# Kernel tuning notes

Measured on AMD Instinct MI355X. Metric: run time of the kernel, lower is better.

The kernel has to match this reference:

```python
import jax, jax.numpy as jnp
import numpy as np

NOISE_STD = 0.01  # noise_std init arg


def setup_inputs() -> dict:
    key = jax.random.key(0)
    k1, k2, k3, k4, k5 = jax.random.split(key, 5)
    B, C, H, W = 32, 256, 56, 56
    x = jax.random.normal(k1, (B, C, H, W), dtype=jnp.float32)
    H_real = jax.random.normal(k2, (B, C, C), dtype=jnp.float32)
    H_imag = jax.random.normal(k3, (B, C, C), dtype=jnp.float32)
    noise_real = jax.random.normal(k4, (B, C, H, W), dtype=jnp.float32)
    noise_imag = jax.random.normal(k5, (B, C, H, W), dtype=jnp.float32)
    return {"x": x, "H_real": H_real, "H_imag": H_imag,
            "noise_real": noise_real, "noise_imag": noise_imag}


def reference(x, H_real, H_imag, noise_real, noise_imag):
    # x: (B,C,H,W) real. Per-batch complex MIMO channel Hc = (Hr + i*Hi)/sqrt(2*C).
    # Since x has zero imaginary part, y = Hc @ x splits into two real GEMMs.
    C = x.shape[1]
    scale = 1.0 / jnp.sqrt(jnp.asarray(2.0 * C, dtype=x.dtype))
    yr = jnp.einsum('bij,bjhw->bihw', H_real, x) * scale + noise_real * NOISE_STD
    yi = jnp.einsum('bij,bjhw->bihw', H_imag, x) * scale + noise_imag * NOISE_STD
    # output_mode == 'magnitude' -> |y|
    return jnp.sqrt(yr * yr + yi * yi)
```

## Files before the change

kernel.cpp:

```cpp
#include <hip/hip_runtime.h>
#include <hip/hip_bf16.h>
#include <math.h>


#define NBATCH 32
#define NC 256
#define NP 3136
#define BM 128
#define BN 64
#define BK 32
#define NBN 49
#define NKI 8

typedef __attribute__((ext_vector_type(8))) short short8;
typedef __attribute__((ext_vector_type(4))) float f32x4;

static __device__ __forceinline__ void gload16(const void* g, void* l) {
  __builtin_amdgcn_global_load_lds(
      (const __attribute__((address_space(1))) void*)g,
      (__attribute__((address_space(3))) void*)l, 16, 0, 0);
}

static __device__ __forceinline__ unsigned short bfr(float f) {
  __hip_bfloat16 h = __float2bfloat16(f);
  return *reinterpret_cast<unsigned short*>(&h);
}

__global__ __launch_bounds__(256)
void perm_h_kernel(const float* __restrict__ hr, const float* __restrict__ hi,
                   unsigned short* __restrict__ ws)
{
  const int blk   = blockIdx.x;
  const int kt    = blk & 7;
  const int b2m   = blk >> 3;
  const int plane = threadIdx.x >> 7;
  const int row   = threadIdx.x & 127;
  const int b     = b2m >> 1;
  const int bm    = b2m & 1;

  const float* src = (plane ? hi : hr)
      + ((size_t)b * NC + bm * 128 + row) * NC + kt * 32;
  unsigned short* dst = ws + ((size_t)(b2m * 8 + kt) * 2 + plane) * 4096 + row * 8;

  #pragma unroll
  for (int fq = 0; fq < 4; ++fq) {
    const float4 v0 = *reinterpret_cast<const float4*>(src + fq * 8);
    const float4 v1 = *reinterpret_cast<const float4*>(src + fq * 8 + 4);
    union { uint4 v; unsigned short u[8]; } o;
    o.u[0] = bfr(v0.x); o.u[1] = bfr(v0.y); o.u[2] = bfr(v0.z); o.u[3] = bfr(v0.w);
    o.u[4] = bfr(v1.x); o.u[5] = bfr(v1.y); o.u[6] = bfr(v1.z); o.u[7] = bfr(v1.w);
    *reinterpret_cast<uint4*>(dst + fq * 1024) = o.v;
  }
}

template<int PRE>
__global__ __launch_bounds__(512, 4)
void rayleigh_main(const float* __restrict__ xg,
                   const float* __restrict__ Hrg,
                   const float* __restrict__ Hig,
                   const unsigned short* __restrict__ Hperm,
                   const float* __restrict__ nrg,
                   const float* __restrict__ nig,
                   float* __restrict__ outg)
{
  __shared__ float x_lds[2][BK * BN];
  __shared__ unsigned short hr_lds[2][4096];
  __shared__ unsigned short hi_lds[2][4096];

  const int raw = blockIdx.x;
  const int v   = (raw & 7) * 392 + (raw >> 3);
  const int b   = v / 98;
  const int r2  = v - b * 98;
  const int bm  = r2 / 49;
  const int bn  = r2 - bm * 49;

  const int tid  = threadIdx.x;
  const int lane = tid & 63;
  const int wave = tid >> 6;
  const int wm   = wave >> 2;
  const int wn   = wave & 3;
  const int fr   = lane & 15;
  const int fq   = lane >> 4;

  const float* xsrc = xg + (size_t)b * NC * NP + (size_t)bn * BN;
  const size_t hrowbase = (size_t)b * NC + bm * BM;
  const size_t hpbase = (size_t)((b * 2 + bm) * 8);

  auto stage = [&](int t, int buf) {
    {
      const int C16 = wave * 64 + lane;
      const int k   = C16 >> 4;
      const int cp  = C16 & 15;
      const int fqk = k >> 3;
      const int cl  = cp ^ (((fqk & 1) << 2) | (fqk >> 1));
      const float* src = xsrc + (size_t)(t * BK + k) * NP + cl * 4;
      gload16(src, (char*)x_lds[buf] + wave * 1024);
    }
    if constexpr (PRE) {
      #pragma unroll
      for (int i = 0; i < 2; ++i) {
        const int c     = wave * 2 + i;
        const int plane = c >> 3;
        const int fqc   = (c >> 1) & 3;
        const int half  = c & 1;
        unsigned short* hl = plane ? hi_lds[buf] : hr_lds[buf];
        const unsigned short* src = Hperm
            + ((hpbase + t) * 2 + plane) * 4096
            + fqc * 1024 + (half * 64 + lane) * 8;
        gload16(src, (char*)hl + fqc * 2048 + half * 1024);
      }
    }
  };

  f32x4 accR[4], accI[4];
  #pragma unroll
  for (int m = 0; m < 4; ++m) {
    accR[m] = (f32x4){0.f, 0.f, 0.f, 0.f};
    accI[m] = (f32x4){0.f, 0.f, 0.f, 0.f};
  }
  float nrv[4][4], niv[4][4];

  const size_t obase = ((size_t)b * NC + bm * BM + wm * 64 + fq * 4) * NP
                     + (size_t)bn * BN + wn * 16 + fr;
  const int xork = ((fq & 1) << 6) | ((fq >> 1) << 4);
  const int pcol = ((wn * 16 + fr) << 2) ^ xork;

  stage(0, 0);

  #pragma unroll
  for (int t = 0; t < NKI; ++t) {
    __syncthreads();
    if (t + 1 < NKI) stage(t + 1, (t + 1) & 1);

    {
      const int m = t >> 1, rb = (t & 1) * 2;
      #pragma unroll
      for (int r = 0; r < 2; ++r) {
        const size_t idx = obase + (size_t)(m * 16 + rb + r) * NP;
        nrv[m][rb + r] = __builtin_nontemporal_load(nrg + idx);
        niv[m][rb + r] = __builtin_nontemporal_load(nig + idx);
      }
    }

    const char* xbuf = (const char*)x_lds[t & 1];
    union { short8 s; unsigned short u[8]; } u;
    #pragma unroll
    for (int j = 0; j < 8; ++j) {
      const float f = *reinterpret_cast<const float*>(xbuf + ((fq * 8 + j) << 8) + pcol);
      u.u[j] = bfr(f);
    }
    const short8 xb = u.s;

    #pragma unroll
    for (int m = 0; m < 4; ++m) {
      const int row = wm * 64 + m * 16 + fr;
      short8 ar, ai;
      if constexpr (PRE) {
        ar = *reinterpret_cast<const short8*>(&hr_lds[t & 1][fq * 1024 + row * 8]);
        ai = *reinterpret_cast<const short8*>(&hi_lds[t & 1][fq * 1024 + row * 8]);
      } else {
        const float* p1 = Hrg + (hrowbase + row) * NC + t * BK + fq * 8;
        const float* p2 = Hig + (hrowbase + row) * NC + t * BK + fq * 8;
        const float4 v0 = *reinterpret_cast<const float4*>(p1);
        const float4 v1 = *reinterpret_cast<const float4*>(p1 + 4);
        const float4 w0 = *reinterpret_cast<const float4*>(p2);
        const float4 w1 = *reinterpret_cast<const float4*>(p2 + 4);
        union { short8 s; unsigned short uu[8]; } a1, a2;
        a1.uu[0] = bfr(v0.x); a1.uu[1] = bfr(v0.y); a1.uu[2] = bfr(v0.z); a1.uu[3] = bfr(v0.w);
        a1.uu[4] = bfr(v1.x); a1.uu[5] = bfr(v1.y); a1.uu[6] = bfr(v1.z); a1.uu[7] = bfr(v1.w);
        a2.uu[0] = bfr(w0.x); a2.uu[1] = bfr(w0.y); a2.uu[2] = bfr(w0.z); a2.uu[3] = bfr(w0.w);
        a2.uu[4] = bfr(w1.x); a2.uu[5] = bfr(w1.y); a2.uu[6] = bfr(w1.z); a2.uu[7] = bfr(w1.w);
        ar = a1.s; ai = a2.s;
      }
      accR[m] = __builtin_amdgcn_mfma_f32_16x16x32_bf16(ar, xb, accR[m], 0, 0, 0);
      accI[m] = __builtin_amdgcn_mfma_f32_16x16x32_bf16(ai, xb, accI[m], 0, 0, 0);
    }
  }

  const float scale = 0.04419417382415922f;
  const float nstd  = 0.01f;
  #pragma unroll
  for (int m = 0; m < 4; ++m)
    #pragma unroll
    for (int r = 0; r < 4; ++r) {
      const size_t idx = obase + (size_t)(m * 16 + r) * NP;
      const float yr = accR[m][r] * scale + nrv[m][r] * nstd;
      const float yi = accI[m][r] * scale + niv[m][r] * nstd;
      outg[idx] = sqrtf(yr * yr + yi * yi);
    }
}

extern "C" void kernel_launch(void* const* d_in, const int* in_sizes, int n_in,
                              void* d_out, int out_size, void* d_ws, size_t ws_size,
                              hipStream_t stream) {
  const float* x  = (const float*)d_in[0];
  const float* Hr = (const float*)d_in[1];
  const float* Hi = (const float*)d_in[2];
  const float* nr = (const float*)d_in[3];
  const float* ni = (const float*)d_in[4];
  float* out = (float*)d_out;

  const size_t HN = (size_t)NBATCH * NC * NC;

  if (ws_size >= HN * 2 * sizeof(unsigned short)) {
    unsigned short* hperm = (unsigned short*)d_ws;
    hipLaunchKernelGGL(perm_h_kernel, dim3(512), dim3(256), 0, stream, Hr, Hi, hperm);
    hipLaunchKernelGGL((rayleigh_main<1>), dim3(NBATCH * 2 * NBN), dim3(512), 0, stream,
                       x, Hr, Hi, hperm, nr, ni, out);
  } else {
    hipLaunchKernelGGL((rayleigh_main<0>), dim3(NBATCH * 2 * NBN), dim3(512), 0, stream,
                       x, Hr, Hi, (const unsigned short*)nullptr, nr, ni, out);
  }
}
```

Baseline: 107.2 us.

## Load full x tile to LDS upfront and stream H from global into registers

Replaces the double-buffered per-K-step LDS staging of x and H with a single upfront load of the whole 256x64 x tile into LDS (64KB) and one barrier. H fragments are now read straight from global memory (L2-cached, prepacked bf16) into registers with an A/B register ping-pong. Noise loads move from interleaved inside the K loop to the epilogue and drop the nontemporal hint. This removes the per-step barriers, but the larger LDS footprint lowers occupancy and the noise load latency is now exposed at the end.

```diff
diff --git a/kernel.cpp b/kernel.cpp
--- a/kernel.cpp
+++ b/kernel.cpp
@@ -63,9 +63,7 @@
                    const float* __restrict__ nig,
                    float* __restrict__ outg)
 {
-  __shared__ float x_lds[2][BK * BN];
-  __shared__ unsigned short hr_lds[2][4096];
-  __shared__ unsigned short hi_lds[2][4096];
+  __shared__ float x_lds[NC * BN];
 
   const int raw = blockIdx.x;
   const int v   = (raw & 7) * 392 + (raw >> 3);
@@ -84,33 +82,17 @@
 
   const float* xsrc = xg + (size_t)b * NC * NP + (size_t)bn * BN;
   const size_t hrowbase = (size_t)b * NC + bm * BM;
-  const size_t hpbase = (size_t)((b * 2 + bm) * 8);
-
-  auto stage = [&](int t, int buf) {
-    {
-      const int C16 = wave * 64 + lane;
-      const int k   = C16 >> 4;
-      const int cp  = C16 & 15;
-      const int fqk = k >> 3;
-      const int cl  = cp ^ (((fqk & 1) << 2) | (fqk >> 1));
-      const float* src = xsrc + (size_t)(t * BK + k) * NP + cl * 4;
-      gload16(src, (char*)x_lds[buf] + wave * 1024);
-    }
-    if constexpr (PRE) {
-      #pragma unroll
-      for (int i = 0; i < 2; ++i) {
-        const int c     = wave * 2 + i;
-        const int plane = c >> 3;
-        const int fqc   = (c >> 1) & 3;
-        const int half  = c & 1;
-        unsigned short* hl = plane ? hi_lds[buf] : hr_lds[buf];
-        const unsigned short* src = Hperm
-            + ((hpbase + t) * 2 + plane) * 4096
-            + fqc * 1024 + (half * 64 + lane) * 8;
-        gload16(src, (char*)hl + fqc * 2048 + half * 1024);
-      }
-    }
-  };
+  const size_t hpbase   = (size_t)((b * 2 + bm) * 8);
+
+  #pragma unroll
+  for (int i = 0; i < 8; ++i) {
+    const int C16 = (i * 8 + wave) * 64 + lane;
+    const int k   = C16 >> 4;
+    const int cp  = C16 & 15;
+    const int fqk = (k >> 3) & 3;
+    const int cl  = cp ^ (((fqk & 1) << 2) | (fqk >> 1));
+    gload16(xsrc + (size_t)k * NP + cl * 4, (char*)x_lds + (i * 8 + wave) * 1024);
+  }
 
   f32x4 accR[4], accI[4];
   #pragma unroll
@@ -118,74 +100,83 @@
     accR[m] = (f32x4){0.f, 0.f, 0.f, 0.f};
     accI[m] = (f32x4){0.f, 0.f, 0.f, 0.f};
   }
-  float nrv[4][4], niv[4][4];
-
-  const size_t obase = ((size_t)b * NC + bm * BM + wm * 64 + fq * 4) * NP
-                     + (size_t)bn * BN + wn * 16 + fr;
+
   const int xork = ((fq & 1) << 6) | ((fq >> 1) << 4);
   const int pcol = ((wn * 16 + fr) << 2) ^ xork;
-
-  stage(0, 0);
-
-  #pragma unroll
-  for (int t = 0; t < NKI; ++t) {
-    __syncthreads();
-    if (t + 1 < NKI) stage(t + 1, (t + 1) & 1);
-
-    {
-      const int m = t >> 1, rb = (t & 1) * 2;
-      #pragma unroll
-      for (int r = 0; r < 2; ++r) {
-        const size_t idx = obase + (size_t)(m * 16 + rb + r) * NP;
-        nrv[m][rb + r] = __builtin_nontemporal_load(nrg + idx);
-        niv[m][rb + r] = __builtin_nontemporal_load(nig + idx);
-      }
-    }
-
-    const char* xbuf = (const char*)x_lds[t & 1];
-    union { short8 s; unsigned short u[8]; } u;
-    #pragma unroll
-    for (int j = 0; j < 8; ++j) {
-      const float f = *reinterpret_cast<const float*>(xbuf + ((fq * 8 + j) << 8) + pcol);
-      u.u[j] = bfr(f);
-    }
-    const short8 xb = u.s;
-
+  const int hfo  = fq * 1024 + (wm * 64 + fr) * 8;
+
+  auto loadH = [&](int t, short8 (&ar)[4], short8 (&ai)[4]) {
     #pragma unroll
     for (int m = 0; m < 4; ++m) {
-      const int row = wm * 64 + m * 16 + fr;
-      short8 ar, ai;
       if constexpr (PRE) {
-        ar = *reinterpret_cast<const short8*>(&hr_lds[t & 1][fq * 1024 + row * 8]);
-        ai = *reinterpret_cast<const short8*>(&hi_lds[t & 1][fq * 1024 + row * 8]);
+        const unsigned short* p = Hperm + ((hpbase + t) * 2) * 4096 + hfo + m * 128;
+        ar[m] = *reinterpret_cast<const short8*>(p);
+        ai[m] = *reinterpret_cast<const short8*>(p + 4096);
       } else {
-        const float* p1 = Hrg + (hrowbase + row) * NC + t * BK + fq * 8;
-        const float* p2 = Hig + (hrowbase + row) * NC + t * BK + fq * 8;
+        const float* p1 = Hrg + (hrowbase + wm * 64 + m * 16 + fr) * NC + t * 32 + fq * 8;
+        const float* p2 = Hig + (hrowbase + wm * 64 + m * 16 + fr) * NC + t * 32 + fq * 8;
         const float4 v0 = *reinterpret_cast<const float4*>(p1);
         const float4 v1 = *reinterpret_cast<const float4*>(p1 + 4);
         const float4 w0 = *reinterpret_cast<const float4*>(p2);
         const float4 w1 = *reinterpret_cast<const float4*>(p2 + 4);
-        union { short8 s; unsigned short uu[8]; } a1, a2;
-        a1.uu[0] = bfr(v0.x); a1.uu[1] = bfr(v0.y); a1.uu[2] = bfr(v0.z); a1.uu[3] = bfr(v0.w);
-        a1.uu[4] = bfr(v1.x); a1.uu[5] = bfr(v1.y); a1.uu[6] = bfr(v1.z); a1.uu[7] = bfr(v1.w);
-        a2.uu[0] = bfr(w0.x); a2.uu[1] = bfr(w0.y); a2.uu[2] = bfr(w0.z); a2.uu[3] = bfr(w0.w);
-        a2.uu[4] = bfr(w1.x); a2.uu[5] = bfr(w1.y); a2.uu[6] = bfr(w1.z); a2.uu[7] = bfr(w1.w);
-        ar = a1.s; ai = a2.s;
+        union { short8 s; unsigned short u[8]; } a1, a2;
+        a1.u[0] = bfr(v0.x); a1.u[1] = bfr(v0.y); a1.u[2] = bfr(v0.z); a1.u[3] = bfr(v0.w);
+        a1.u[4] = bfr(v1.x); a1.u[5] = bfr(v1.y); a1.u[6] = bfr(v1.z); a1.u[7] = bfr(v1.w);
+        a2.u[0] = bfr(w0.x); a2.u[1] = bfr(w0.y); a2.u[2] = bfr(w0.z); a2.u[3] = bfr(w0.w);
+        a2.u[4] = bfr(w1.x); a2.u[5] = bfr(w1.y); a2.u[6] = bfr(w1.z); a2.u[7] = bfr(w1.w);
+        ar[m] = a1.s; ai[m] = a2.s;
       }
-      accR[m] = __builtin_amdgcn_mfma_f32_16x16x32_bf16(ar, xb, accR[m], 0, 0, 0);
-      accI[m] = __builtin_amdgcn_mfma_f32_16x16x32_bf16(ai, xb, accI[m], 0, 0, 0);
-    }
+    }
+  };
+
+  auto step = [&](int t, short8 (&ar)[4], short8 (&ai)[4]) {
+    union { short8 s; unsigned short u[8]; } u;
+    #pragma unroll
+    for (int j = 0; j < 8; ++j) {
+      const float f = *reinterpret_cast<const float*>(
+          (const char*)x_lds + ((t * 32 + fq * 8 + j) << 8) + pcol);
+      u.u[j] = bfr(f);
+    }
+    const short8 xb = u.s;
+    #pragma unroll
+    for (int m = 0; m < 4; ++m) {
+      accR[m] = __builtin_amdgcn_mfma_f32_16x16x32_bf16(ar[m], xb, accR[m], 0, 0, 0);
+      accI[m] = __builtin_amdgcn_mfma_f32_16x16x32_bf16(ai[m], xb, accI[m], 0, 0, 0);
+    }
+  };
+
+  short8 arA[4], aiA[4], arB[4], aiB[4];
+  loadH(0, arA, aiA);
+  __syncthreads();
+
+  #pragma unroll
+  for (int u2 = 0; u2 < 4; ++u2) {
+    loadH(2 * u2 + 1, arB, aiB);
+    step(2 * u2, arA, aiA);
+    if (u2 < 3) loadH(2 * u2 + 2, arA, aiA);
+    step(2 * u2 + 1, arB, aiB);
   }
 
   const float scale = 0.04419417382415922f;
   const float nstd  = 0.01f;
+  const size_t obase = ((size_t)b * NC + bm * BM + wm * 64 + fq * 4) * NP
+                     + (size_t)bn * BN + wn * 16 + fr;
+  float nrv[16], niv[16];
   #pragma unroll
   for (int m = 0; m < 4; ++m)
     #pragma unroll
     for (int r = 0; r < 4; ++r) {
       const size_t idx = obase + (size_t)(m * 16 + r) * NP;
-      const float yr = accR[m][r] * scale + nrv[m][r] * nstd;
-      const float yi = accI[m][r] * scale + niv[m][r] * nstd;
+      nrv[m * 4 + r] = nrg[idx];
+      niv[m * 4 + r] = nig[idx];
+    }
+  #pragma unroll
+  for (int m = 0; m < 4; ++m)
+    #pragma unroll
+    for (int r = 0; r < 4; ++r) {
+      const size_t idx = obase + (size_t)(m * 16 + r) * NP;
+      const float yr = accR[m][r] * scale + nrv[m * 4 + r] * nstd;
+      const float yi = accI[m][r] * scale + niv[m * 4 + r] * nstd;
       outg[idx] = sqrtf(yr * yr + yi * yi);
     }
 }
```

After: 133.0 us. 24.0% more time.

## Triple-buffer LDS staging with manual vmcnt waits and move noise loads to epilogue

Applied to the files above, without the earlier changes.

Switches the K-loop from double to triple buffering with a prefetch distance of two. It replaces __syncthreads with an explicit s_waitcnt vmcnt plus s_barrier so that in-flight global-to-LDS loads can overlap compute. The noise loads, which were interleaved into the K loop as nontemporal loads, now all issue in the epilogue as ordinary loads. This frees the loop's vmcnt accounting but exposes noise load latency at the end, and the extra LDS buffer may cut occupancy.

```diff
diff --git a/kernel.cpp b/kernel.cpp
--- a/kernel.cpp
+++ b/kernel.cpp
@@ -63,9 +63,9 @@
                    const float* __restrict__ nig,
                    float* __restrict__ outg)
 {
-  __shared__ float x_lds[2][BK * BN];
-  __shared__ unsigned short hr_lds[2][4096];
-  __shared__ unsigned short hi_lds[2][4096];
+  __shared__ float x_lds[3][BK * BN];
+  __shared__ unsigned short hr_lds[3][4096];
+  __shared__ unsigned short hi_lds[3][4096];
 
   const int raw = blockIdx.x;
   const int v   = (raw & 7) * 392 + (raw >> 3);
@@ -84,7 +84,7 @@
 
   const float* xsrc = xg + (size_t)b * NC * NP + (size_t)bn * BN;
   const size_t hrowbase = (size_t)b * NC + bm * BM;
-  const size_t hpbase = (size_t)((b * 2 + bm) * 8);
+  const size_t hpbase   = (size_t)((b * 2 + bm) * 8);
 
   auto stage = [&](int t, int buf) {
     {
@@ -118,7 +118,6 @@
     accR[m] = (f32x4){0.f, 0.f, 0.f, 0.f};
     accI[m] = (f32x4){0.f, 0.f, 0.f, 0.f};
   }
-  float nrv[4][4], niv[4][4];
 
   const size_t obase = ((size_t)b * NC + bm * BM + wm * 64 + fq * 4) * NP
                      + (size_t)bn * BN + wn * 16 + fr;
@@ -126,23 +125,21 @@
   const int pcol = ((wn * 16 + fr) << 2) ^ xork;
 
   stage(0, 0);
-
-  #pragma unroll
+  stage(1, 1);
+
   for (int t = 0; t < NKI; ++t) {
-    __syncthreads();
-    if (t + 1 < NKI) stage(t + 1, (t + 1) & 1);
-
-    {
-      const int m = t >> 1, rb = (t & 1) * 2;
-      #pragma unroll
-      for (int r = 0; r < 2; ++r) {
-        const size_t idx = obase + (size_t)(m * 16 + rb + r) * NP;
-        nrv[m][rb + r] = __builtin_nontemporal_load(nrg + idx);
-        niv[m][rb + r] = __builtin_nontemporal_load(nig + idx);
-      }
-    }
-
-    const char* xbuf = (const char*)x_lds[t & 1];
+    const int buf = t % 3;
+    if constexpr (PRE) {
+      if (t < NKI - 1) asm volatile("s_waitcnt vmcnt(3)" ::: "memory");
+      else             asm volatile("s_waitcnt vmcnt(0)" ::: "memory");
+      __builtin_amdgcn_s_barrier();
+      __builtin_amdgcn_sched_barrier(0);
+    } else {
+      __syncthreads();
+    }
+    if (t + 2 < NKI) stage(t + 2, (t + 2) % 3);
+
+    const char* xbuf = (const char*)x_lds[buf];
     union { short8 s; unsigned short u[8]; } u;
     #pragma unroll
     for (int j = 0; j < 8; ++j) {
@@ -156,11 +153,11 @@
       const int row = wm * 64 + m * 16 + fr;
       short8 ar, ai;
       if constexpr (PRE) {
-        ar = *reinterpret_cast<const short8*>(&hr_lds[t & 1][fq * 1024 + row * 8]);
-        ai = *reinterpret_cast<const short8*>(&hi_lds[t & 1][fq * 1024 + row * 8]);
+        ar = *reinterpret_cast<const short8*>(&hr_lds[buf][fq * 1024 + row * 8]);
+        ai = *reinterpret_cast<const short8*>(&hi_lds[buf][fq * 1024 + row * 8]);
       } else {
-        const float* p1 = Hrg + (hrowbase + row) * NC + t * BK + fq * 8;
-        const float* p2 = Hig + (hrowbase + row) * NC + t * BK + fq * 8;
+        const float* p1 = Hrg + (hrowbase + row) * NC + t * 32 + fq * 8;
+        const float* p2 = Hig + (hrowbase + row) * NC + t * 32 + fq * 8;
         const float4 v0 = *reinterpret_cast<const float4*>(p1);
         const float4 v1 = *reinterpret_cast<const float4*>(p1 + 4);
         const float4 w0 = *reinterpret_cast<const float4*>(p2);
@@ -179,13 +176,22 @@
 
   const float scale = 0.04419417382415922f;
   const float nstd  = 0.01f;
+  float nrv[16], niv[16];
   #pragma unroll
   for (int m = 0; m < 4; ++m)
     #pragma unroll
     for (int r = 0; r < 4; ++r) {
       const size_t idx = obase + (size_t)(m * 16 + r) * NP;
-      const float yr = accR[m][r] * scale + nrv[m][r] * nstd;
-      const float yi = accI[m][r] * scale + niv[m][r] * nstd;
+      nrv[m * 4 + r] = nrg[idx];
+      niv[m * 4 + r] = nig[idx];
+    }
+  #pragma unroll
+  for (int m = 0; m < 4; ++m)
+    #pragma unroll
+    for (int r = 0; r < 4; ++r) {
+      const size_t idx = obase + (size_t)(m * 16 + r) * NP;
+      const float yr = accR[m][r] * scale + nrv[m * 4 + r] * nstd;
+      const float yi = accI[m][r] * scale + niv[m * 4 + r] * nstd;
       outg[idx] = sqrtf(yr * yr + yi * yi);
     }
 }
```

Result: slower. 111.9 us (+4.4%).

## Cover full channel dimension per block so x tile is loaded once

Applied to the files above, without the earlier changes.

Enlarges the M tile from 128 to 256 rows so each block computes all output channels for its pixel tile. Each x tile is now read from global memory once instead of twice, and the grid shrinks to 1568 blocks. Each wave handles two N sub-tiles, which doubles the accumulators and the LDS for H. The noise loads move out of the K loop into the epilogue and output stores become nontemporal. The risk is fewer resident blocks from higher register and LDS use, and noise-load latency no longer hidden behind the main loop.

```diff
diff --git a/kernel.cpp b/kernel.cpp
--- a/kernel.cpp
+++ b/kernel.cpp
@@ -6,7 +6,7 @@
 #define NBATCH 32
 #define NC 256
 #define NP 3136
-#define BM 128
+#define BM 256
 #define BN 64
 #define BK 32
 #define NBN 49
@@ -64,27 +64,25 @@
                    float* __restrict__ outg)
 {
   __shared__ float x_lds[2][BK * BN];
-  __shared__ unsigned short hr_lds[2][4096];
-  __shared__ unsigned short hi_lds[2][4096];
+  __shared__ unsigned short hr_lds[2][8192];
+  __shared__ unsigned short hi_lds[2][8192];
 
   const int raw = blockIdx.x;
-  const int v   = (raw & 7) * 392 + (raw >> 3);
-  const int b   = v / 98;
-  const int r2  = v - b * 98;
-  const int bm  = r2 / 49;
-  const int bn  = r2 - bm * 49;
+  const int v   = (raw & 7) * 196 + (raw >> 3);
+  const int b   = v / NBN;
+  const int bn  = v - b * NBN;
 
   const int tid  = threadIdx.x;
   const int lane = tid & 63;
   const int wave = tid >> 6;
-  const int wm   = wave >> 2;
-  const int wn   = wave & 3;
+  const int wm   = wave >> 1;
+  const int wn   = wave & 1;
   const int fr   = lane & 15;
   const int fq   = lane >> 4;
 
   const float* xsrc = xg + (size_t)b * NC * NP + (size_t)bn * BN;
-  const size_t hrowbase = (size_t)b * NC + bm * BM;
-  const size_t hpbase = (size_t)((b * 2 + bm) * 8);
+  const size_t hrowbase = (size_t)b * NC;
+  const size_t hpb      = (size_t)(b * 2) * 8;
 
   auto stage = [&](int t, int buf) {
     {
@@ -98,32 +96,32 @@
     }
     if constexpr (PRE) {
       #pragma unroll
-      for (int i = 0; i < 2; ++i) {
-        const int c     = wave * 2 + i;
-        const int plane = c >> 3;
-        const int fqc   = (c >> 1) & 3;
-        const int half  = c & 1;
+      for (int i = 0; i < 4; ++i) {
+        const int c     = wave * 4 + i;
+        const int plane = c >> 4;
+        const int c4    = c & 15;
+        const int bm2   = c4 >> 3;
+        const int fqc   = (c4 >> 1) & 3;
+        const int half  = c4 & 1;
         unsigned short* hl = plane ? hi_lds[buf] : hr_lds[buf];
         const unsigned short* src = Hperm
-            + ((hpbase + t) * 2 + plane) * 4096
+            + (((hpb + bm2 * 8 + t) * 2) + plane) * 4096
             + fqc * 1024 + (half * 64 + lane) * 8;
-        gload16(src, (char*)hl + fqc * 2048 + half * 1024);
+        gload16(src, (char*)hl + fqc * 4096 + bm2 * 2048 + half * 1024);
       }
     }
   };
 
-  f32x4 accR[4], accI[4];
-  #pragma unroll
-  for (int m = 0; m < 4; ++m) {
-    accR[m] = (f32x4){0.f, 0.f, 0.f, 0.f};
-    accI[m] = (f32x4){0.f, 0.f, 0.f, 0.f};
-  }
-  float nrv[4][4], niv[4][4];
-
-  const size_t obase = ((size_t)b * NC + bm * BM + wm * 64 + fq * 4) * NP
-                     + (size_t)bn * BN + wn * 16 + fr;
+  f32x4 accR[4][2], accI[4][2];
+  #pragma unroll
+  for (int m = 0; m < 4; ++m)
+    #pragma unroll
+    for (int n = 0; n < 2; ++n) {
+      accR[m][n] = (f32x4){0.f, 0.f, 0.f, 0.f};
+      accI[m][n] = (f32x4){0.f, 0.f, 0.f, 0.f};
+    }
+
   const int xork = ((fq & 1) << 6) | ((fq >> 1) << 4);
-  const int pcol = ((wn * 16 + fr) << 2) ^ xork;
 
   stage(0, 0);
 
@@ -132,35 +130,30 @@
     __syncthreads();
     if (t + 1 < NKI) stage(t + 1, (t + 1) & 1);
 
-    {
-      const int m = t >> 1, rb = (t & 1) * 2;
-      #pragma unroll
-      for (int r = 0; r < 2; ++r) {
-        const size_t idx = obase + (size_t)(m * 16 + rb + r) * NP;
-        nrv[m][rb + r] = __builtin_nontemporal_load(nrg + idx);
-        niv[m][rb + r] = __builtin_nontemporal_load(nig + idx);
-      }
-    }
-
     const char* xbuf = (const char*)x_lds[t & 1];
-    union { short8 s; unsigned short u[8]; } u;
-    #pragma unroll
-    for (int j = 0; j < 8; ++j) {
-      const float f = *reinterpret_cast<const float*>(xbuf + ((fq * 8 + j) << 8) + pcol);
-      u.u[j] = bfr(f);
-    }
-    const short8 xb = u.s;
+    short8 xb[2];
+    #pragma unroll
+    for (int n = 0; n < 2; ++n) {
+      const int pcol = ((wn * 32 + n * 16 + fr) << 2) ^ xork;
+      union { short8 s; unsigned short u[8]; } u;
+      #pragma unroll
+      for (int j = 0; j < 8; ++j) {
+        const float f = *reinterpret_cast<const float*>(xbuf + ((fq * 8 + j) << 8) + pcol);
+        u.u[j] = bfr(f);
+      }
+      xb[n] = u.s;
+    }
 
     #pragma unroll
     for (int m = 0; m < 4; ++m) {
       const int row = wm * 64 + m * 16 + fr;
       short8 ar, ai;
       if constexpr (PRE) {
-        ar = *reinterpret_cast<const short8*>(&hr_lds[t & 1][fq * 1024 + row * 8]);
-        ai = *reinterpret_cast<const short8*>(&hi_lds[t & 1][fq * 1024 + row * 8]);
+        ar = *reinterpret_cast<const short8*>(&hr_lds[t & 1][fq * 2048 + row * 8]);
+        ai = *reinterpret_cast<const short8*>(&hi_lds[t & 1][fq * 2048 + row * 8]);
       } else {
-        const float* p1 = Hrg + (hrowbase + row) * NC + t * BK + fq * 8;
-        const float* p2 = Hig + (hrowbase + row) * NC + t * BK + fq * 8;
+        const float* p1 = Hrg + (hrowbase + row) * NC + t * 32 + fq * 8;
+        const float* p2 = Hig + (hrowbase + row) * NC + t * 32 + fq * 8;
         const float4 v0 = *reinterpret_cast<const float4*>(p1);
         const float4 v1 = *reinterpret_cast<const float4*>(p1 + 4);
         const float4 w0 = *reinterpret_cast<const float4*>(p2);
@@ -172,21 +165,36 @@
         a2.uu[4] = bfr(w1.x); a2.uu[5] = bfr(w1.y); a2.uu[6] = bfr(w1.z); a2.uu[7] = bfr(w1.w);
         ar = a1.s; ai = a2.s;
       }
-      accR[m] = __builtin_amdgcn_mfma_f32_16x16x32_bf16(ar, xb, accR[m], 0, 0, 0);
-      accI[m] = __builtin_amdgcn_mfma_f32_16x16x32_bf16(ai, xb, accI[m], 0, 0, 0);
+      #pragma unroll
+      for (int n = 0; n < 2; ++n) {
+        accR[m][n] = __builtin_amdgcn_mfma_f32_16x16x32_bf16(ar, xb[n], accR[m][n], 0, 0, 0);
+        accI[m][n] = __builtin_amdgcn_mfma_f32_16x16x32_bf16(ai, xb[n], accI[m][n], 0, 0, 0);
+      }
     }
   }
 
   const float scale = 0.04419417382415922f;
   const float nstd  = 0.01f;
+  const size_t obase = ((size_t)b * NC + wm * 64 + fq * 4) * NP
+                     + (size_t)bn * BN + wn * 32 + fr;
   #pragma unroll
   for (int m = 0; m < 4; ++m)
     #pragma unroll
-    for (int r = 0; r < 4; ++r) {
-      const size_t idx = obase + (size_t)(m * 16 + r) * NP;
-      const float yr = accR[m][r] * scale + nrv[m][r] * nstd;
-      const float yi = accI[m][r] * scale + niv[m][r] * nstd;
-      outg[idx] = sqrtf(yr * yr + yi * yi);
+    for (int n = 0; n < 2; ++n) {
+      float nrv[4], niv[4];
+      #pragma unroll
+      for (int r = 0; r < 4; ++r) {
+        const size_t idx = obase + (size_t)(m * 16 + r) * NP + n * 16;
+        nrv[r] = nrg[idx];
+        niv[r] = nig[idx];
+      }
+      #pragma unroll
+      for (int r = 0; r < 4; ++r) {
+        const size_t idx = obase + (size_t)(m * 16 + r) * NP + n * 16;
+        const float yr = accR[m][n][r] * scale + nrv[r] * nstd;
+        const float yi = accI[m][n][r] * scale + niv[r] * nstd;
+        __builtin_nontemporal_store(sqrtf(yr * yr + yi * yi), outg + idx);
+      }
     }
 }
 
@@ -205,10 +213,10 @@
   if (ws_size >= HN * 2 * sizeof(unsigned short)) {
     unsigned short* hperm = (unsigned short*)d_ws;
     hipLaunchKernelGGL(perm_h_kernel, dim3(512), dim3(256), 0, stream, Hr, Hi, hperm);
-    hipLaunchKernelGGL((rayleigh_main<1>), dim3(NBATCH * 2 * NBN), dim3(512), 0, stream,
+    hipLaunchKernelGGL((rayleigh_main<1>), dim3(NBATCH * NBN), dim3(512), 0, stream,
                        x, Hr, Hi, hperm, nr, ni, out);
   } else {
-    hipLaunchKernelGGL((rayleigh_main<0>), dim3(NBATCH * 2 * NBN), dim3(512), 0, stream,
+    hipLaunchKernelGGL((rayleigh_main<0>), dim3(NBATCH * NBN), dim3(512), 0, stream,
                        x, Hr, Hi, (const unsigned short*)nullptr, nr, ni, out);
   }
 }
```

Measured after the change: 130.6 us. 1.22x slower.
